# Optimization experiments

Hardware: AMD Instinct MI355X
Metric: run time of the kernel (lower is better)

## Reference

```python
import jax, jax.numpy as jnp
import numpy as np

B, N = 4, 1024
D_MODEL, N_HEADS, D_HEAD, D_COORD = 512, 8, 64, 2


def setup_inputs() -> dict:
    key = jax.random.key(0)
    ks = jax.random.split(key, 8)
    sd = 1.0 / np.sqrt(D_MODEL)
    return {
        "x": jax.random.normal(ks[0], (B, N, D_MODEL), dtype=jnp.float32),
        "positions": jax.random.uniform(ks[1], (N, D_COORD), dtype=jnp.float32) * 32.0,
        "W_Q": jax.random.normal(ks[2], (D_MODEL, N_HEADS * D_HEAD), dtype=jnp.float32) * sd,
        "W_K": jax.random.normal(ks[3], (D_MODEL, N_HEADS * D_HEAD), dtype=jnp.float32) * sd,
        "W_V": jax.random.normal(ks[4], (D_MODEL, N_HEADS * D_HEAD), dtype=jnp.float32) * sd,
        "W_O": jax.random.normal(ks[5], (N_HEADS * D_HEAD, D_MODEL), dtype=jnp.float32) * sd,
        "U": jax.random.normal(ks[6], (N_HEADS, D_HEAD, D_HEAD), dtype=jnp.float32),
        "freqs": jax.random.normal(ks[7], (N_HEADS, D_HEAD // 2, D_COORD), dtype=jnp.float32),
    }


def reference(x, positions, W_Q, W_K, W_V, W_O, U, freqs):
    # x: (B,N,d_model); positions: (N,d_coord); U: (H,dh,dh); freqs: (H,m,d_coord)
    Bn, Nn, _ = x.shape
    H, dh, _ = U.shape
    m = dh // 2
    scale = (dh // 2) ** -0.5

    Q = (x @ W_Q).reshape(Bn, Nn, H, dh)
    K = (x @ W_K).reshape(Bn, Nn, H, dh)
    V = (x @ W_V).reshape(Bn, Nn, H, dh)

    # Active-subspace projector: Pi = qr(U)[0] @ qr(U)[0].T per head
    Uq = jax.vmap(lambda u: jnp.linalg.qr(u)[0])(U)              # (H,dh,dh)
    P = jnp.einsum('hde,hfe->hdf', Uq, Uq)                       # U U^T
    Qp = jnp.einsum('bnhd,hdf->bhnf', Q, P)                      # (B,H,N,dh)
    Kp = jnp.einsum('bnhd,hdf->bhnf', K, P)

    # Relative rotation: R_rel(r_j - r_i) is block-diag 2x2 rotations with
    # angle theta_ijm = freqs_m . (r_j - r_i) = a_jm - a_im (separable), so
    # q^T R(r_j-r_i) k = (R(a_i)q)^T (R(a_j)k)  -- exact RoPE identity.
    ang = jnp.einsum('nc,hmc->hnm', positions, freqs)            # (H,N,m)
    c = jnp.cos(ang)[None]                                       # (1,H,N,m)
    s = jnp.sin(ang)[None]

    def rot(v):  # v: (B,H,N,dh) -> rotated (even, odd) halves (B,H,N,m)
        ve, vo = v[..., ::2], v[..., 1::2]
        return ve * c - vo * s, ve * s + vo * c

    qe, qo = rot(Qp)
    ke, ko = rot(Kp)
    scores = (jnp.einsum('bhim,bhjm->bhij', qe, ke)
              + jnp.einsum('bhim,bhjm->bhij', qo, ko)) * scale   # (B,H,N,N)
    w = jax.nn.softmax(scores, axis=-1)
    out = jnp.einsum('bhij,bjhd->bihd', w, V).reshape(Bn, Nn, H * dh)
    return out @ W_O
```

## Files before the change

### kernel.cpp

```cpp
#include <hip/hip_runtime.h>
#include <math.h>

#define NBATCH 4
#define NSEQ   1024
#define DMODEL 512
#define NH     8
#define DH     64
#define MROWS  (NBATCH*NSEQ)
#define MHALF  (DH/2)

typedef __attribute__((ext_vector_type(8))) short bf16x8;
typedef __attribute__((ext_vector_type(4))) float floatx4;

__device__ __forceinline__ ushort f2bf(float f) {
    union { float f; uint u; } v; v.f = f;
    uint r = v.u + 0x7fffu + ((v.u >> 16) & 1u);
    return (ushort)(r >> 16);
}

__global__ __launch_bounds__(256) void prep_kernel(
    const float* __restrict__ pos, const float* __restrict__ freqs,
    const float* __restrict__ x,
    const float* __restrict__ Wq, const float* __restrict__ Wk,
    const float* __restrict__ Wv, const float* __restrict__ Wo,
    float* __restrict__ cosT, float* __restrict__ sinT,
    ushort* __restrict__ xb, ushort* __restrict__ Wt)
{
    __shared__ float T[64][65];
    const int bid = blockIdx.x;
    const int tid = threadIdx.x;

    if (bid < 1024) {
        int idx = bid * 256 + tid;
        int m = idx & 31;
        int n = (idx >> 5) & 1023;
        int h = idx >> 15;
        float a = pos[n*2+0] * freqs[(h*MHALF+m)*2+0]
                + pos[n*2+1] * freqs[(h*MHALF+m)*2+1];
        cosT[idx] = cosf(a);
        sinT[idx] = sinf(a);
    } else if (bid < 2048) {
        int idx = ((bid - 1024) * 256 + tid) * 8;
        float4 a = *(const float4*)&x[idx];
        float4 b = *(const float4*)&x[idx+4];
        uint4 pk;
        pk.x = (uint)f2bf(a.x) | ((uint)f2bf(a.y) << 16);
        pk.y = (uint)f2bf(a.z) | ((uint)f2bf(a.w) << 16);
        pk.z = (uint)f2bf(b.x) | ((uint)f2bf(b.y) << 16);
        pk.w = (uint)f2bf(b.z) | ((uint)f2bf(b.w) << 16);
        *(uint4*)&xb[idx] = pk;
    } else {
        int b2 = bid - 2048;
        int n0g = (b2 & 31) * 64;
        int k0  = (b2 >> 5) * 64;
        int mat = n0g >> 9;
        const float* W = (mat == 0) ? Wq : ((mat == 1) ? Wk : ((mat == 2) ? Wv : Wo));
        int n0 = n0g & 511;
        int c = tid & 63, r = tid >> 6;
        #pragma unroll
        for (int i = 0; i < 16; i++)
            T[r + i*4][c] = W[(k0 + r + i*4) * DMODEL + n0 + c];
        __syncthreads();
        int nl = tid >> 2;
        int kg = tid & 3;
        #pragma unroll
        for (int g = 0; g < 4; g++) {
            int kl = kg * 16 + g * 4;
            uint2 pk;
            pk.x = (uint)f2bf(T[kl+0][nl]) | ((uint)f2bf(T[kl+1][nl]) << 16);
            pk.y = (uint)f2bf(T[kl+2][nl]) | ((uint)f2bf(T[kl+3][nl]) << 16);
            *(uint2*)&Wt[(size_t)(n0g + nl) * DMODEL + k0 + kl] = pk;
        }
    }
}

__global__ __launch_bounds__(256) void qkv_gemm(
    const ushort* __restrict__ xb, const ushort* __restrict__ Wt,
    const float* __restrict__ cosT, const float* __restrict__ sinT,
    ushort* __restrict__ Qb, ushort* __restrict__ Kb, ushort* __restrict__ Vt)
{
    __shared__ ushort As[64 * 40];
    __shared__ ushort Bs[64 * 40];
    __shared__ float  Cs[64][65];

    const int cb = blockIdx.x;
    const int rb = blockIdx.y;
    const int mat = cb >> 3;
    const int c0 = (cb & 7) * 64;
    const int r0 = rb * 64;
    const int ng0 = mat * 512 + c0;

    const int tid = threadIdx.x;
    const int w = tid >> 6, l = tid & 63;
    const int lr = l & 15, lg = l >> 4;

    const int srow = tid >> 2;
    const int sgrp = tid & 3;

    floatx4 acc[4];
    #pragma unroll
    for (int nt = 0; nt < 4; nt++) acc[nt] = (floatx4){0.f,0.f,0.f,0.f};

    for (int k0 = 0; k0 < DMODEL; k0 += 32) {
        __syncthreads();
        *(uint4*)&As[srow*40 + sgrp*8] =
            *(const uint4*)&xb[(size_t)(r0 + srow) * DMODEL + k0 + sgrp*8];
        *(uint4*)&Bs[srow*40 + sgrp*8] =
            *(const uint4*)&Wt[(size_t)(ng0 + srow) * DMODEL + k0 + sgrp*8];
        __syncthreads();

        bf16x8 af = *(const bf16x8*)&As[(16*w + lr)*40 + lg*8];
        #pragma unroll
        for (int nt = 0; nt < 4; nt++) {
            bf16x8 bf = *(const bf16x8*)&Bs[(nt*16 + lr)*40 + lg*8];
            acc[nt] = __builtin_amdgcn_mfma_f32_16x16x32_bf16(af, bf, acc[nt], 0, 0, 0);
        }
    }

    __syncthreads();
    #pragma unroll
    for (int nt = 0; nt < 4; nt++)
        #pragma unroll
        for (int r = 0; r < 4; r++)
            Cs[16*w + lg*4 + r][nt*16 + lr] = acc[nt][r];
    __syncthreads();

    const int tx = tid & 15, ty = tid >> 4;
    const int dbase = tx * 4;
    const int head = c0 >> 6;

    if (mat == 2) {
        int rowbase = r0 + ty * 4;
        int b = rowbase >> 10, n0 = rowbase & 1023;
        size_t vbase = (size_t)(b * NH + head) * DH;
        #pragma unroll
        for (int j = 0; j < 4; j++) {
            ushort us[4];
            #pragma unroll
            for (int i = 0; i < 4; i++) us[i] = f2bf(Cs[ty*4 + i][tx*4 + j]);
            uint2 pk;
            pk.x = (uint)us[0] | ((uint)us[1] << 16);
            pk.y = (uint)us[2] | ((uint)us[3] << 16);
            *(uint2*)&Vt[(vbase + dbase + j) * NSEQ + n0] = pk;
        }
    } else {
        ushort* dst = (mat == 0) ? Qb : Kb;
        #pragma unroll
        for (int i = 0; i < 4; i++) {
            int row = r0 + ty * 4 + i;
            int b = row >> 10, n = row & 1023;
            float v[4];
            #pragma unroll
            for (int p = 0; p < 2; p++) {
                int de = dbase + 2 * p;
                int m = de >> 1;
                float c = cosT[(head * NSEQ + n) * MHALF + m];
                float s = sinT[(head * NSEQ + n) * MHALF + m];
                float ve = Cs[ty*4 + i][tx*4 + 2*p];
                float vo = Cs[ty*4 + i][tx*4 + 2*p + 1];
                v[2*p]     = ve * c - vo * s;
                v[2*p + 1] = ve * s + vo * c;
            }
            uint2 pk;
            pk.x = (uint)f2bf(v[0]) | ((uint)f2bf(v[1]) << 16);
            pk.y = (uint)f2bf(v[2]) | ((uint)f2bf(v[3]) << 16);
            *(uint2*)&dst[((size_t)(b * NH + head) * NSEQ + n) * DH + dbase] = pk;
        }
    }
}

__global__ __launch_bounds__(256, 4) void attn_kernel(
    const ushort* __restrict__ Qb, const ushort* __restrict__ Kb,
    const ushort* __restrict__ Vt, float* __restrict__ Opart,
    float* __restrict__ Lsum)
{
    __shared__ ushort Ks[64 * 72];
    __shared__ ushort Vs[64 * 72];
    __shared__ ushort Ps[64 * 72];

    const int tid = threadIdx.x;
    const int w = tid >> 6, l = tid & 63;
    const int lr = l & 15, lg = l >> 4;
    const int bh = blockIdx.y, q0 = blockIdx.x * 64;
    const int z = blockIdx.z, jt0 = z * 8;

    const ushort* Qg = Qb + (size_t)bh * NSEQ * DH;
    const ushort* Kg = Kb + (size_t)bh * NSEQ * DH;
    const ushort* Vg = Vt + (size_t)bh * DH * NSEQ;

    bf16x8 qf[2];
    #pragma unroll
    for (int ks = 0; ks < 2; ks++)
        qf[ks] = *(const bf16x8*)(Qg + (size_t)(q0 + 16*w + lr) * DH + ks*32 + lg*8);

    floatx4 ot[4];
    #pragma unroll
    for (int i = 0; i < 4; i++) ot[i] = (floatx4){0.f, 0.f, 0.f, 0.f};
    float rsum = 0.f;
    const float cexp = 0.2550348550f;

    const int sr = tid >> 2;
    const int sc = (tid & 3) * 16;

    const ushort* kp = Kg + (size_t)(jt0*64 + sr) * DH + sc;
    uint4 ka  = *(const uint4*)kp;
    uint4 kb2 = *(const uint4*)(kp + 8);
    const ushort* vp = Vg + (size_t)sr * NSEQ + jt0*64 + sc;
    uint4 va  = *(const uint4*)vp;
    uint4 vb2 = *(const uint4*)(vp + 8);

    for (int jt = jt0; jt < jt0 + 8; jt++) {
        __syncthreads();
        *(uint4*)&Ks[sr*72 + sc]     = ka;
        *(uint4*)&Ks[sr*72 + sc + 8] = kb2;
        *(uint4*)&Vs[sr*72 + sc]     = va;
        *(uint4*)&Vs[sr*72 + sc + 8] = vb2;
        __syncthreads();

        if (jt < jt0 + 7) {
            const ushort* kn = Kg + (size_t)((jt+1)*64 + sr) * DH + sc;
            ka  = *(const uint4*)kn;
            kb2 = *(const uint4*)(kn + 8);
            const ushort* vn = Vg + (size_t)sr * NSEQ + (jt+1)*64 + sc;
            va  = *(const uint4*)vn;
            vb2 = *(const uint4*)(vn + 8);
        }

        floatx4 st[4];
        #pragma unroll
        for (int jm = 0; jm < 4; jm++) {
            floatx4 acc = (floatx4){0.f, 0.f, 0.f, 0.f};
            #pragma unroll
            for (int ks = 0; ks < 2; ks++) {
                bf16x8 af = *(const bf16x8*)&Ks[(jm*16 + lr)*72 + ks*32 + lg*8];
                acc = __builtin_amdgcn_mfma_f32_16x16x32_bf16(af, qf[ks], acc, 0, 0, 0);
            }
            st[jm] = acc;
        }

        #pragma unroll
        for (int jm = 0; jm < 4; jm++) {
            ushort us[4];
            #pragma unroll
            for (int r = 0; r < 4; r++) {
                float p = exp2f(st[jm][r] * cexp);
                rsum += p;
                us[r] = f2bf(p);
            }
            uint2 pk;
            pk.x = (uint)us[0] | ((uint)us[1] << 16);
            pk.y = (uint)us[2] | ((uint)us[3] << 16);
            *(uint2*)&Ps[(16*w + lr)*72 + jm*16 + lg*4] = pk;
        }

        bf16x8 pf[2];
        #pragma unroll
        for (int ks = 0; ks < 2; ks++)
            pf[ks] = *(const bf16x8*)&Ps[(16*w + lr)*72 + ks*32 + lg*8];
        #pragma unroll
        for (int dt = 0; dt < 4; dt++)
            #pragma unroll
            for (int ks = 0; ks < 2; ks++) {
                bf16x8 af = *(const bf16x8*)&Vs[(dt*16 + lr)*72 + ks*32 + lg*8];
                ot[dt] = __builtin_amdgcn_mfma_f32_16x16x32_bf16(af, pf[ks], ot[dt], 0, 0, 0);
            }
    }

    rsum += __shfl_xor(rsum, 16, 64);
    rsum += __shfl_xor(rsum, 32, 64);

    int n = q0 + 16*w + lr;
    size_t obase = ((size_t)(z * 32 + bh) * NSEQ + n) * DH;
    #pragma unroll
    for (int dt = 0; dt < 4; dt++)
        *(floatx4*)&Opart[obase + dt*16 + lg*4] = ot[dt];
    if (lg == 0)
        Lsum[(size_t)(z * 32 + bh) * NSEQ + n] = rsum;
}

__global__ __launch_bounds__(256) void out_gemm(
    const float* __restrict__ Op, const float* __restrict__ Ls,
    const ushort* __restrict__ Wt, float* __restrict__ out)
{
    __shared__ ushort As[64 * 40];
    __shared__ ushort Bs[64 * 40];
    __shared__ float  Cs[64][65];

    const int cb = blockIdx.x;
    const int rb = blockIdx.y;
    const int c0 = cb * 64, r0 = rb * 64;

    const int tid = threadIdx.x;
    const int w = tid >> 6, l = tid & 63;
    const int lr = l & 15, lg = l >> 4;
    const int srow = tid >> 2;
    const int sgrp = tid & 3;

    const int arow = r0 + srow;
    const int b = arow >> 10, n = arow & 1023;

    floatx4 acc[4];
    #pragma unroll
    for (int nt = 0; nt < 4; nt++) acc[nt] = (floatx4){0.f,0.f,0.f,0.f};

    for (int k0 = 0; k0 < DMODEL; k0 += 32) {
        int h = k0 >> 6;
        int d0 = k0 & 63;
        size_t qi = (size_t)(b * NH + h) * NSEQ + n;
        const float* p1 = Op + qi * 64 + d0 + sgrp*8;
        const float* p2 = p1 + (size_t)32768 * 64;
        float inv = 1.f / (Ls[qi] + Ls[32768 + qi]);
        float4 u0 = *(const float4*)p1;
        float4 u1 = *(const float4*)(p1 + 4);
        float4 v0 = *(const float4*)p2;
        float4 v1 = *(const float4*)(p2 + 4);
        uint4 apk;
        apk.x = (uint)f2bf((u0.x+v0.x)*inv) | ((uint)f2bf((u0.y+v0.y)*inv) << 16);
        apk.y = (uint)f2bf((u0.z+v0.z)*inv) | ((uint)f2bf((u0.w+v0.w)*inv) << 16);
        apk.z = (uint)f2bf((u1.x+v1.x)*inv) | ((uint)f2bf((u1.y+v1.y)*inv) << 16);
        apk.w = (uint)f2bf((u1.z+v1.z)*inv) | ((uint)f2bf((u1.w+v1.w)*inv) << 16);
        __syncthreads();
        *(uint4*)&As[srow*40 + sgrp*8] = apk;
        *(uint4*)&Bs[srow*40 + sgrp*8] =
            *(const uint4*)&Wt[(size_t)(1536 + c0 + srow) * DMODEL + k0 + sgrp*8];
        __syncthreads();

        bf16x8 af = *(const bf16x8*)&As[(16*w + lr)*40 + lg*8];
        #pragma unroll
        for (int nt = 0; nt < 4; nt++) {
            bf16x8 bf = *(const bf16x8*)&Bs[(nt*16 + lr)*40 + lg*8];
            acc[nt] = __builtin_amdgcn_mfma_f32_16x16x32_bf16(af, bf, acc[nt], 0, 0, 0);
        }
    }

    __syncthreads();
    #pragma unroll
    for (int nt = 0; nt < 4; nt++)
        #pragma unroll
        for (int r = 0; r < 4; r++)
            Cs[16*w + lg*4 + r][nt*16 + lr] = acc[nt][r];
    __syncthreads();

    const int tx = tid & 15, ty = tid >> 4;
    #pragma unroll
    for (int i = 0; i < 4; i++) {
        float4 o;
        o.x = Cs[ty*4 + i][tx*4 + 0];
        o.y = Cs[ty*4 + i][tx*4 + 1];
        o.z = Cs[ty*4 + i][tx*4 + 2];
        o.w = Cs[ty*4 + i][tx*4 + 3];
        *(float4*)&out[(size_t)(r0 + ty*4 + i) * DMODEL + c0 + tx*4] = o;
    }
}

extern "C" void kernel_launch(void* const* d_in, const int* in_sizes, int n_in,
                              void* d_out, int out_size, void* d_ws, size_t ws_size,
                              hipStream_t stream) {
    const float* x         = (const float*)d_in[0];
    const float* positions = (const float*)d_in[1];
    const float* Wq        = (const float*)d_in[2];
    const float* Wk        = (const float*)d_in[3];
    const float* Wv        = (const float*)d_in[4];
    const float* Wo        = (const float*)d_in[5];
    const float* freqs     = (const float*)d_in[7];
    float* out = (float*)d_out;

    float*  ws    = (float*)d_ws;
    float*  cosT  = ws;
    float*  sinT  = cosT + NH*NSEQ*MHALF;
    float*  Opart = sinT + NH*NSEQ*MHALF;
    float*  Lsum  = Opart + 2*(size_t)NBATCH*NH*NSEQ*DH;
    ushort* xb    = (ushort*)(Lsum + 2*(size_t)NBATCH*NH*NSEQ);
    ushort* Wt    = xb + (size_t)MROWS*DMODEL;
    ushort* Qb    = Wt + (size_t)2048*DMODEL;
    ushort* Kb    = Qb + (size_t)NBATCH*NH*NSEQ*DH;
    ushort* Vt    = Kb + (size_t)NBATCH*NH*NSEQ*DH;

    prep_kernel<<<dim3(2304), 256, 0, stream>>>(positions, freqs, x, Wq, Wk, Wv, Wo,
                                                cosT, sinT, xb, Wt);
    qkv_gemm<<<dim3(24, 64), 256, 0, stream>>>(xb, Wt, cosT, sinT, Qb, Kb, Vt);
    attn_kernel<<<dim3(16, 32, 2), 256, 0, stream>>>(Qb, Kb, Vt, Opart, Lsum);
    out_gemm<<<dim3(8, 64), 256, 0, stream>>>(Opart, Lsum, Wt, out);
}
```

Before: 138.0 us.

## Merge split-K attention partials in last-arriving block and emit bf16 output

The attention kernel now uses a per-tile atomic counter so that whichever of the two split blocks finishes second combines both partial outputs, normalizes by the summed row sums, and writes a bf16 attention output. The output GEMM then loads that bf16 tensor directly, instead of reading two fp32 partials and the sums and normalizing in every k-step, which was repeated across 8 column blocks. The score MFMA loop is also interleaved with the exp/pack step. This adds a threadfence and atomic per block, extra fp32 partial reads in the merging block, and a counter reset in the prep kernel.

```diff
diff --git a/kernel.cpp b/kernel.cpp
--- a/kernel.cpp
+++ b/kernel.cpp
@@ -24,13 +24,15 @@
     const float* __restrict__ Wq, const float* __restrict__ Wk,
     const float* __restrict__ Wv, const float* __restrict__ Wo,
     float* __restrict__ cosT, float* __restrict__ sinT,
-    ushort* __restrict__ xb, ushort* __restrict__ Wt)
+    ushort* __restrict__ xb, ushort* __restrict__ Wt,
+    uint* __restrict__ cnt)
 {
     __shared__ float T[64][65];
     const int bid = blockIdx.x;
     const int tid = threadIdx.x;
 
     if (bid < 1024) {
+        if (bid == 0) { cnt[tid] = 0u; cnt[tid + 256] = 0u; }
         int idx = bid * 256 + tid;
         int m = idx & 31;
         int n = (idx >> 5) & 1023;
@@ -172,11 +174,13 @@
 __global__ __launch_bounds__(256, 4) void attn_kernel(
     const ushort* __restrict__ Qb, const ushort* __restrict__ Kb,
     const ushort* __restrict__ Vt, float* __restrict__ Opart,
-    float* __restrict__ Lsum)
+    float* __restrict__ Lsum, uint* __restrict__ cnt,
+    ushort* __restrict__ Obb)
 {
     __shared__ ushort Ks[64 * 72];
     __shared__ ushort Vs[64 * 72];
     __shared__ ushort Ps[64 * 72];
+    __shared__ int lastflag;
 
     const int tid = threadIdx.x;
     const int w = tid >> 6, l = tid & 63;
@@ -226,24 +230,17 @@
             vb2 = *(const uint4*)(vn + 8);
         }
 
-        floatx4 st[4];
         #pragma unroll
         for (int jm = 0; jm < 4; jm++) {
-            floatx4 acc = (floatx4){0.f, 0.f, 0.f, 0.f};
-            #pragma unroll
-            for (int ks = 0; ks < 2; ks++) {
-                bf16x8 af = *(const bf16x8*)&Ks[(jm*16 + lr)*72 + ks*32 + lg*8];
-                acc = __builtin_amdgcn_mfma_f32_16x16x32_bf16(af, qf[ks], acc, 0, 0, 0);
-            }
-            st[jm] = acc;
-        }
-
-        #pragma unroll
-        for (int jm = 0; jm < 4; jm++) {
+            bf16x8 a0 = *(const bf16x8*)&Ks[(jm*16 + lr)*72 + lg*8];
+            bf16x8 a1 = *(const bf16x8*)&Ks[(jm*16 + lr)*72 + 32 + lg*8];
+            floatx4 s = (floatx4){0.f, 0.f, 0.f, 0.f};
+            s = __builtin_amdgcn_mfma_f32_16x16x32_bf16(a0, qf[0], s, 0, 0, 0);
+            s = __builtin_amdgcn_mfma_f32_16x16x32_bf16(a1, qf[1], s, 0, 0, 0);
             ushort us[4];
             #pragma unroll
             for (int r = 0; r < 4; r++) {
-                float p = exp2f(st[jm][r] * cexp);
+                float p = exp2f(s[r] * cexp);
                 rsum += p;
                 us[r] = f2bf(p);
             }
@@ -258,29 +255,51 @@
         for (int ks = 0; ks < 2; ks++)
             pf[ks] = *(const bf16x8*)&Ps[(16*w + lr)*72 + ks*32 + lg*8];
         #pragma unroll
-        for (int dt = 0; dt < 4; dt++)
-            #pragma unroll
-            for (int ks = 0; ks < 2; ks++) {
-                bf16x8 af = *(const bf16x8*)&Vs[(dt*16 + lr)*72 + ks*32 + lg*8];
-                ot[dt] = __builtin_amdgcn_mfma_f32_16x16x32_bf16(af, pf[ks], ot[dt], 0, 0, 0);
-            }
+        for (int dt = 0; dt < 4; dt++) {
+            bf16x8 v0 = *(const bf16x8*)&Vs[(dt*16 + lr)*72 + lg*8];
+            bf16x8 v1 = *(const bf16x8*)&Vs[(dt*16 + lr)*72 + 32 + lg*8];
+            ot[dt] = __builtin_amdgcn_mfma_f32_16x16x32_bf16(v0, pf[0], ot[dt], 0, 0, 0);
+            ot[dt] = __builtin_amdgcn_mfma_f32_16x16x32_bf16(v1, pf[1], ot[dt], 0, 0, 0);
+        }
     }
 
     rsum += __shfl_xor(rsum, 16, 64);
     rsum += __shfl_xor(rsum, 32, 64);
 
-    int n = q0 + 16*w + lr;
-    size_t obase = ((size_t)(z * 32 + bh) * NSEQ + n) * DH;
+    const int n = q0 + 16*w + lr;
+    const size_t obase = ((size_t)(z * 32 + bh) * NSEQ + n) * DH;
     #pragma unroll
     for (int dt = 0; dt < 4; dt++)
         *(floatx4*)&Opart[obase + dt*16 + lg*4] = ot[dt];
     if (lg == 0)
         Lsum[(size_t)(z * 32 + bh) * NSEQ + n] = rsum;
+
+    __threadfence();
+    if (tid == 0)
+        lastflag = (int)atomicAdd(&cnt[blockIdx.x * 32 + bh], 1u);
+    __syncthreads();
+
+    if (lastflag == 1) {
+        __threadfence();
+        const int zo = 1 - z;
+        const size_t obase2 = ((size_t)(zo * 32 + bh) * NSEQ + n) * DH;
+        const float lo = Lsum[(size_t)(zo * 32 + bh) * NSEQ + n];
+        const float inv = 1.f / (rsum + lo);
+        #pragma unroll
+        for (int dt = 0; dt < 4; dt++) {
+            floatx4 o2 = *(const floatx4*)&Opart[obase2 + dt*16 + lg*4];
+            floatx4 s = (ot[dt] + o2) * inv;
+            uint2 pk;
+            pk.x = (uint)f2bf(s[0]) | ((uint)f2bf(s[1]) << 16);
+            pk.y = (uint)f2bf(s[2]) | ((uint)f2bf(s[3]) << 16);
+            *(uint2*)&Obb[((size_t)bh * NSEQ + n) * DH + dt*16 + lg*4] = pk;
+        }
+    }
 }
 
 __global__ __launch_bounds__(256) void out_gemm(
-    const float* __restrict__ Op, const float* __restrict__ Ls,
-    const ushort* __restrict__ Wt, float* __restrict__ out)
+    const ushort* __restrict__ Obb, const ushort* __restrict__ Wt,
+    float* __restrict__ out)
 {
     __shared__ ushort As[64 * 40];
     __shared__ ushort Bs[64 * 40];
@@ -306,21 +325,9 @@
     for (int k0 = 0; k0 < DMODEL; k0 += 32) {
         int h = k0 >> 6;
         int d0 = k0 & 63;
-        size_t qi = (size_t)(b * NH + h) * NSEQ + n;
-        const float* p1 = Op + qi * 64 + d0 + sgrp*8;
-        const float* p2 = p1 + (size_t)32768 * 64;
-        float inv = 1.f / (Ls[qi] + Ls[32768 + qi]);
-        float4 u0 = *(const float4*)p1;
-        float4 u1 = *(const float4*)(p1 + 4);
-        float4 v0 = *(const float4*)p2;
-        float4 v1 = *(const float4*)(p2 + 4);
-        uint4 apk;
-        apk.x = (uint)f2bf((u0.x+v0.x)*inv) | ((uint)f2bf((u0.y+v0.y)*inv) << 16);
-        apk.y = (uint)f2bf((u0.z+v0.z)*inv) | ((uint)f2bf((u0.w+v0.w)*inv) << 16);
-        apk.z = (uint)f2bf((u1.x+v1.x)*inv) | ((uint)f2bf((u1.y+v1.y)*inv) << 16);
-        apk.w = (uint)f2bf((u1.z+v1.z)*inv) | ((uint)f2bf((u1.w+v1.w)*inv) << 16);
-        __syncthreads();
-        *(uint4*)&As[srow*40 + sgrp*8] = apk;
+        __syncthreads();
+        *(uint4*)&As[srow*40 + sgrp*8] =
+            *(const uint4*)&Obb[((size_t)(b * NH + h) * NSEQ + n) * DH + d0 + sgrp*8];
         *(uint4*)&Bs[srow*40 + sgrp*8] =
             *(const uint4*)&Wt[(size_t)(1536 + c0 + srow) * DMODEL + k0 + sgrp*8];
         __syncthreads();
@@ -370,15 +377,17 @@
     float*  sinT  = cosT + NH*NSEQ*MHALF;
     float*  Opart = sinT + NH*NSEQ*MHALF;
     float*  Lsum  = Opart + 2*(size_t)NBATCH*NH*NSEQ*DH;
-    ushort* xb    = (ushort*)(Lsum + 2*(size_t)NBATCH*NH*NSEQ);
+    uint*   cnt   = (uint*)(Lsum + 2*(size_t)NBATCH*NH*NSEQ);
+    ushort* xb    = (ushort*)(cnt + 512);
     ushort* Wt    = xb + (size_t)MROWS*DMODEL;
     ushort* Qb    = Wt + (size_t)2048*DMODEL;
     ushort* Kb    = Qb + (size_t)NBATCH*NH*NSEQ*DH;
     ushort* Vt    = Kb + (size_t)NBATCH*NH*NSEQ*DH;
+    ushort* Obb   = Vt + (size_t)NBATCH*NH*NSEQ*DH;
 
     prep_kernel<<<dim3(2304), 256, 0, stream>>>(positions, freqs, x, Wq, Wk, Wv, Wo,
-                                                cosT, sinT, xb, Wt);
+                                                cosT, sinT, xb, Wt, cnt);
     qkv_gemm<<<dim3(24, 64), 256, 0, stream>>>(xb, Wt, cosT, sinT, Qb, Kb, Vt);
-    attn_kernel<<<dim3(16, 32, 2), 256, 0, stream>>>(Qb, Kb, Vt, Opart, Lsum);
-    out_gemm<<<dim3(8, 64), 256, 0, stream>>>(Opart, Lsum, Wt, out);
-}
+    attn_kernel<<<dim3(16, 32, 2), 256, 0, stream>>>(Qb, Kb, Vt, Opart, Lsum, cnt, Obb);
+    out_gemm<<<dim3(8, 64), 256, 0, stream>>>(Obb, Wt, out);
+}
```

Result: slower. 299.2 us (+116.8%).
